# Kernel tuning notes

Measured on AMD Instinct MI355X. Metric: run time of the kernel, lower is better.

## Reference

```python
import jax, jax.numpy as jnp
import numpy as np
import math

E = 256      # emb_size
H = 4        # num_heads
D = E // H   # head_dim
EXPLORE_SCALE = 0.5
EXPLOIT_SCALE = 0.5
TEMP_MIN = 0.5
TEMP_MAX = 2.0


def setup_inputs() -> dict:
    key = jax.random.key(0)
    ks = jax.random.split(key, 12)
    B, S = 4, 2048
    his_emb = jax.random.normal(ks[0], (B, S, E), dtype=jnp.float32)
    src_key_padding_mask = jax.random.randint(ks[1], (B, S), 0, 2) > 0
    explore = jax.random.uniform(ks[2], (B, S), dtype=jnp.float32)
    exploit = jax.random.uniform(ks[3], (B, S), dtype=jnp.float32)
    scale = 1.0 / math.sqrt(E)
    Wq = jax.random.normal(ks[4], (E, E), dtype=jnp.float32) * scale
    bq = jnp.zeros((E,), dtype=jnp.float32)
    Wk = jax.random.normal(ks[5], (E, E), dtype=jnp.float32) * scale
    bk = jnp.zeros((E,), dtype=jnp.float32)
    Wv = jax.random.normal(ks[6], (E, E), dtype=jnp.float32) * scale
    bv = jnp.zeros((E,), dtype=jnp.float32)
    Wo = jax.random.normal(ks[7], (E, E), dtype=jnp.float32) * scale
    bo = jnp.zeros((E,), dtype=jnp.float32)
    return {"his_emb": his_emb, "src_key_padding_mask": src_key_padding_mask,
            "explore": explore, "exploit": exploit,
            "Wq": Wq, "bq": bq, "Wk": Wk, "bk": bk,
            "Wv": Wv, "bv": bv, "Wo": Wo, "bo": bo}


def reference(his_emb, src_key_padding_mask, explore, exploit,
              Wq, bq, Wk, bk, Wv, bv, Wo, bo):
    B, S, _ = his_emb.shape
    # projections -> [B, H, S, D]
    q = (his_emb @ Wq + bq).reshape(B, S, H, D).transpose(0, 2, 1, 3)
    k = (his_emb @ Wk + bk).reshape(B, S, H, D).transpose(0, 2, 1, 3)
    v = (his_emb @ Wv + bv).reshape(B, S, H, D).transpose(0, 2, 1, 3)
    logits = jnp.einsum('bhqd,bhkd->bhqk', q, k) / math.sqrt(D)
    attn_mask = src_key_padding_mask[:, None, None, :]  # [B,1,1,S] over keys
    logits = jnp.where(attn_mask, -1e16, logits)
    # per-query dynamic temperature
    temp = 1.0 + EXPLORE_SCALE * explore - EXPLOIT_SCALE * exploit  # [B,S]
    temp = jnp.clip(temp, TEMP_MIN, TEMP_MAX)
    temp = jnp.where(src_key_padding_mask, 1.0, temp)
    logits = logits / temp[:, None, :, None]
    probs = jax.nn.softmax(logits, axis=-1)
    probs = jnp.where(attn_mask, 0.0, probs)
    probs = probs / jnp.maximum(probs.sum(axis=-1, keepdims=True), 1e-8)
    out = jnp.einsum('bhqk,bhkd->bhqd', probs, v)
    out = out.transpose(0, 2, 1, 3).reshape(B, S, E)
    out = out @ Wo + bo
    return jnp.where(src_key_padding_mask[:, :, None], 0.0, out)
```

## Files before the change

kernel.cpp:

```cpp
#include <hip/hip_runtime.h>
#include <math.h>

#define B_ 4
#define S_ 2048
#define E_ 256
#define H_ 4
#define D_ 64
#define NROW (B_*S_)
#define NCH 2
#define CHK (S_/NCH)
#define NT (CHK/64)
#define LOG2E 1.4426950408889634f
#define NFM  (-17.312340490667562f)

typedef __attribute__((ext_vector_type(8)))  short short8;
typedef __attribute__((ext_vector_type(4)))  float floatx4;
typedef __attribute__((ext_vector_type(16))) float floatx16;

__device__ __forceinline__ short f2bf(float f){
    union{float f; unsigned u;} x; x.f = f;
    unsigned r = x.u + 0x7fffu + ((x.u>>16)&1u);
    return (short)(r>>16);
}
__device__ __forceinline__ unsigned cvtpk(float a, float b){
    unsigned r; asm("v_cvt_pk_bf16_f32 %0, %1, %2" : "=v"(r) : "v"(a), "v"(b)); return r;
}

__global__ __launch_bounds__(256) void prep(
    const float* __restrict__ W0, const float* __restrict__ W1,
    const float* __restrict__ W2, const float* __restrict__ W3,
    const float* __restrict__ X,
    short* __restrict__ T0, short* __restrict__ T1,
    short* __restrict__ T2, short* __restrict__ T3,
    short* __restrict__ Xb)
{
    __shared__ float L[64][65];
    const int t = threadIdx.x;
    if (blockIdx.x >= 16){
        const int cid = (blockIdx.x - 16) + 128*blockIdx.y;
        const float4* src = (const float4*)(X + (size_t)cid*4096 + t*16);
        short8 o0, o1; float4 u;
        u = src[0]; o0[0]=f2bf(u.x); o0[1]=f2bf(u.y); o0[2]=f2bf(u.z); o0[3]=f2bf(u.w);
        u = src[1]; o0[4]=f2bf(u.x); o0[5]=f2bf(u.y); o0[6]=f2bf(u.z); o0[7]=f2bf(u.w);
        u = src[2]; o1[0]=f2bf(u.x); o1[1]=f2bf(u.y); o1[2]=f2bf(u.z); o1[3]=f2bf(u.w);
        u = src[3]; o1[4]=f2bf(u.x); o1[5]=f2bf(u.y); o1[6]=f2bf(u.z); o1[7]=f2bf(u.w);
        short* dst = Xb + (size_t)cid*4096 + t*16;
        *(short8*)dst = o0; *(short8*)(dst+8) = o1;
        return;
    }
    const float* W = blockIdx.y==0?W0: blockIdx.y==1?W1: blockIdx.y==2?W2:W3;
    short*       T = blockIdx.y==0?T0: blockIdx.y==1?T1: blockIdx.y==2?T2:T3;
    const int k0 = (blockIdx.x>>2)*64, n0 = (blockIdx.x&3)*64;
    {
        int r = t>>2, c0 = (t&3)*16;
        const float4* p = (const float4*)(W + (size_t)(k0+r)*E_ + n0 + c0);
        #pragma unroll
        for (int j=0;j<4;++j){
            float4 u = p[j];
            L[r][c0+4*j]=u.x; L[r][c0+4*j+1]=u.y; L[r][c0+4*j+2]=u.z; L[r][c0+4*j+3]=u.w;
        }
    }
    __syncthreads();
    {
        int n = t>>2, kk0 = (t&3)*16;
        short8 o0, o1;
        #pragma unroll
        for(int j=0;j<8;++j) o0[j] = f2bf(L[kk0+j][n]);
        #pragma unroll
        for(int j=0;j<8;++j) o1[j] = f2bf(L[kk0+8+j][n]);
        short* dst = T + (size_t)(n0+n)*E_ + k0 + kk0;
        *(short8*)dst = o0; *(short8*)(dst+8) = o1;
    }
}

__global__ __launch_bounds__(256) void qkv_gemm(
    const short* __restrict__ Xb,
    const short* __restrict__ Wtq, const float* __restrict__ bq,
    const short* __restrict__ Wtk, const float* __restrict__ bk,
    const short* __restrict__ Wtv, const float* __restrict__ bv,
    short* __restrict__ Q, short* __restrict__ K, short* __restrict__ Vt)
{
    const int z = blockIdx.z;
    const short* Wt   = z==0?Wtq: z==1?Wtk:Wtv;
    const float* bias = z==0?bq:  z==1?bk:bv;

    __shared__ __align__(16) short As[64][72];
    __shared__ __align__(16) short Bs[64][72];

    const int t=threadIdx.x, w=t>>6, lane=t&63, ln=lane&15, quad=lane>>4;
    const int m0 = blockIdx.y*64, n0 = blockIdx.x*64;

    floatx4 acc[4] = {};
    for (int kt=0; kt<E_; kt+=64){
        __syncthreads();
        {
            int r=t>>2, c0=(t&3)*16;
            const uint4* pa = (const uint4*)(Xb + (size_t)(m0+r)*E_ + kt + c0);
            *(uint4*)&As[r][c0] = pa[0]; *(uint4*)&As[r][c0+8] = pa[1];
            const uint4* pb = (const uint4*)(Wt + (size_t)(n0+r)*E_ + kt + c0);
            *(uint4*)&Bs[r][c0] = pb[0]; *(uint4*)&Bs[r][c0+8] = pb[1];
        }
        __syncthreads();
        short8 a0 = *(const short8*)&As[w*16+ln][quad*8];
        short8 a1 = *(const short8*)&As[w*16+ln][32+quad*8];
        #pragma unroll
        for (int c=0;c<4;++c){
            short8 b0 = *(const short8*)&Bs[c*16+ln][quad*8];
            short8 b1 = *(const short8*)&Bs[c*16+ln][32+quad*8];
            acc[c] = __builtin_amdgcn_mfma_f32_16x16x32_bf16(a0,b0,acc[c],0,0,0);
            acc[c] = __builtin_amdgcn_mfma_f32_16x16x32_bf16(a1,b1,acc[c],0,0,0);
        }
    }
    if (z<2){
        short* dst = z==0?Q:K;
        #pragma unroll
        for(int c=0;c<4;++c){
            int colg = n0 + c*16 + ln;
            float bia = bias[colg];
            #pragma unroll
            for(int reg=0;reg<4;++reg){
                int row = m0 + w*16 + quad*4 + reg;
                dst[(size_t)row*E_ + colg] = f2bf(acc[c][reg] + bia);
            }
        }
    } else {
        #pragma unroll
        for(int c=0;c<4;++c){
            int colg = n0 + c*16 + ln;
            int hx = colg>>6, d = colg&63;
            float bia = bias[colg];
            #pragma unroll
            for(int reg=0;reg<4;++reg){
                int row = m0 + w*16 + quad*4 + reg;
                int bb = row>>11, s = row&(S_-1);
                Vt[((size_t)((bb*H_+hx)*D_+d))*S_ + s] = f2bf(acc[c][reg] + bia);
            }
        }
    }
}

__global__ __launch_bounds__(256) void attn_mfma(
    const short* __restrict__ Qb, const short* __restrict__ Kb, const short* __restrict__ Vtb,
    const int* __restrict__ mask,
    const float* __restrict__ explore, const float* __restrict__ exploit,
    float* __restrict__ OP, float* __restrict__ Lb)
{
    const int bid = blockIdx.x + 16*blockIdx.y + 32*blockIdx.z;
    const int swz = (bid & 7)*64 + (bid >> 3);
    const int bx = swz & 15;
    const int ck = (swz >> 4) & 1;
    const int z  = swz >> 5;
    const int b = z >> 2, h = z & 3;
    const int q0 = bx*128;
    const int k0 = ck*CHK;

    const int t = threadIdx.x, w = t>>6, lane = t&63, l31 = lane&31, hi = lane>>5;

    __shared__ __align__(16) short Ks[2][64][72];
    __shared__ __align__(16) short Vs[2][64][72];
    __shared__ float mb[2][64];

    const int qbase = q0 + w*32;
    const int qg = qbase + l31;
    float tsc2;
    {
        float ex = explore[b*S_+qg], xp = exploit[b*S_+qg];
        float tmp = fminf(fmaxf(1.0f + 0.5f*ex - 0.5f*xp, 0.5f), 2.0f);
        if (mask[b*S_+qg]) tmp = 1.0f;
        tsc2 = LOG2E/(tmp*8.0f);
    }
    const size_t qrow = (size_t)(b*S_+qg)*E_ + h*D_ + hi*8;
    const short8 qf0 = *(const short8*)(Qb + qrow);
    const short8 qf1 = *(const short8*)(Qb + qrow + 16);
    const short8 qf2 = *(const short8*)(Qb + qrow + 32);
    const short8 qf3 = *(const short8*)(Qb + qrow + 48);

    floatx16 ofa = {}, ofb = {};
    float lacc = 0.0f;

    const int sr = t>>2, sc = (t&3)*16;
    const short* kgp = Kb  + (size_t)(b*S_)*E_ + h*D_ + sc;
    const short* vgp = Vtb + ((size_t)(b*H_+h)*D_ + sr)*S_;

    uint4 rk0, rk1, rv0, rv1; float mfv = 0.0f;
    {
        const uint4* gk = (const uint4*)(kgp + (size_t)(k0+sr)*E_);
        rk0 = gk[0]; rk1 = gk[1];
        const uint4* gv = (const uint4*)(vgp + k0 + sc);
        rv0 = gv[0]; rv1 = gv[1];
        if (t < 64) mfv = mask[b*S_ + k0 + t] ? -1e30f : NFM;
    }
    *(uint4*)&Ks[0][sr][sc] = rk0; *(uint4*)&Ks[0][sr][sc+8] = rk1;
    *(uint4*)&Vs[0][sr][sc] = rv0; *(uint4*)&Vs[0][sr][sc+8] = rv1;
    if (t < 64) mb[0][t] = mfv;
    {
        const uint4* gk = (const uint4*)(kgp + (size_t)(k0+64+sr)*E_);
        rk0 = gk[0]; rk1 = gk[1];
        const uint4* gv = (const uint4*)(vgp + k0 + 64 + sc);
        rv0 = gv[0]; rv1 = gv[1];
        if (t < 64) mfv = mask[b*S_ + k0 + 64 + t] ? -1e30f : NFM;
    }
    __syncthreads();

    int cur = 0;
    #pragma unroll 1
    for (int it = 0; it < NT; ++it){
        const short (*Kc)[72] = Ks[cur];
        const short (*Vc)[72] = Vs[cur];
        #pragma unroll
        for (int kg = 0; kg < 2; ++kg){
            floatx16 st = {};
            const short8 kf0 = *(const short8*)&Kc[kg*32+l31][hi*8];
            const short8 kf1 = *(const short8*)&Kc[kg*32+l31][16+hi*8];
            const short8 kf2 = *(const short8*)&Kc[kg*32+l31][32+hi*8];
            const short8 kf3 = *(const short8*)&Kc[kg*32+l31][48+hi*8];
            __builtin_amdgcn_s_setprio(1);
            st = __builtin_amdgcn_mfma_f32_32x32x16_bf16(kf0, qf0, st, 0,0,0);
            st = __builtin_amdgcn_mfma_f32_32x32x16_bf16(kf1, qf1, st, 0,0,0);
            st = __builtin_amdgcn_mfma_f32_32x32x16_bf16(kf2, qf2, st, 0,0,0);
            st = __builtin_amdgcn_mfma_f32_32x32x16_bf16(kf3, qf3, st, 0,0,0);
            __builtin_amdgcn_s_setprio(0);
            const float4 m0_ = *(const float4*)&mb[cur][kg*32 +      4*hi];
            const float4 m1_ = *(const float4*)&mb[cur][kg*32 +  8 + 4*hi];
            const float4 m2_ = *(const float4*)&mb[cur][kg*32 + 16 + 4*hi];
            const float4 m3_ = *(const float4*)&mb[cur][kg*32 + 24 + 4*hi];
            const float mbf[16] = {m0_.x,m0_.y,m0_.z,m0_.w, m1_.x,m1_.y,m1_.z,m1_.w,
                                   m2_.x,m2_.y,m2_.z,m2_.w, m3_.x,m3_.y,m3_.z,m3_.w};
            float p[16];
            #pragma unroll
            for (int r = 0; r < 16; ++r){
                p[r] = __builtin_amdgcn_exp2f(st[r]*tsc2 + mbf[r]);
                lacc += p[r];
            }
            #pragma unroll
            for (int c = 0; c < 2; ++c){
                unsigned w0 = cvtpk(p[c*8+0], p[c*8+1]);
                unsigned w1 = cvtpk(p[c*8+2], p[c*8+3]);
                unsigned w2 = cvtpk(p[c*8+4], p[c*8+5]);
                unsigned w3 = cvtpk(p[c*8+6], p[c*8+7]);
                asm("v_permlane32_swap_b32 %0, %1" : "+v"(w0), "+v"(w2));
                asm("v_permlane32_swap_b32 %0, %1" : "+v"(w1), "+v"(w3));
                union { uint4 u; short8 s; } pc;
                pc.u.x = w0; pc.u.y = w1; pc.u.z = w2; pc.u.w = w3;
                const short8 vf0 = *(const short8*)&Vc[l31]   [kg*32 + c*16 + hi*8];
                const short8 vf1 = *(const short8*)&Vc[32+l31][kg*32 + c*16 + hi*8];
                __builtin_amdgcn_s_setprio(1);
                ofa = __builtin_amdgcn_mfma_f32_32x32x16_bf16(pc.s, vf0, ofa, 0,0,0);
                ofb = __builtin_amdgcn_mfma_f32_32x32x16_bf16(pc.s, vf1, ofb, 0,0,0);
                __builtin_amdgcn_s_setprio(0);
            }
        }
        if (it + 1 < NT){
            *(uint4*)&Ks[cur^1][sr][sc] = rk0; *(uint4*)&Ks[cur^1][sr][sc+8] = rk1;
            *(uint4*)&Vs[cur^1][sr][sc] = rv0; *(uint4*)&Vs[cur^1][sr][sc+8] = rv1;
            if (t < 64) mb[cur^1][t] = mfv;
            if (it + 2 < NT){
                const int kt2 = k0 + (it+2)*64;
                const uint4* gk = (const uint4*)(kgp + (size_t)(kt2+sr)*E_);
                rk0 = gk[0]; rk1 = gk[1];
                const uint4* gv = (const uint4*)(vgp + kt2 + sc);
                rv0 = gv[0]; rv1 = gv[1];
                if (t < 64) mfv = mask[b*S_ + kt2 + t] ? -1e30f : NFM;
            }
        }
        __syncthreads();
        cur ^= 1;
    }

    const float l = lacc + __shfl_xor(lacc, 32);
    const size_t obase = ((size_t)(ck*B_+b)*H_+h)*S_;
    if (hi == 0) Lb[obase + qg] = l;
    #pragma unroll
    for (int r = 0; r < 16; ++r){
        const int q = qbase + (r&3) + 8*(r>>2) + 4*hi;
        float* dst = OP + (obase + q)*D_;
        dst[l31]      = ofa[r];
        dst[32 + l31] = ofb[r];
    }
}

__global__ __launch_bounds__(256) void out_gemm(
    const float* __restrict__ OP, const float* __restrict__ Lb,
    const short* __restrict__ Wto, const float* __restrict__ bo,
    const int* __restrict__ mask, float* __restrict__ out)
{
    __shared__ __align__(16) short As[64][72];
    __shared__ __align__(16) short Bs[64][72];
    const int bid = blockIdx.x + 4*blockIdx.y;
    const int swz = (bid & 7)*64 + (bid >> 3);
    const int n0 = (swz & 3)*64;
    const int m0 = (swz >> 2)*64;
    const int t=threadIdx.x, w=t>>6, lane=t&63, ln=lane&15, quad=lane>>4;
    floatx4 acc[4] = {};
    const int sr=t>>2, sc=(t&3)*16;
    const int rowg = m0 + sr, bb = rowg>>11, ss = rowg&(S_-1);
    #pragma unroll 1
    for (int kt=0; kt<E_; kt+=64){
        const int hx = kt>>6;
        const size_t r0 = ((size_t)(bb)*H_+hx)*S_+ss;
        const size_t r1 = ((size_t)(B_+bb)*H_+hx)*S_+ss;
        const float lsum = Lb[r0] + Lb[r1];
        const float rl = 1.0f/fmaxf(lsum, 1e-8f);
        const float* pa0 = OP + r0*D_ + sc;
        const float* pa1 = OP + r1*D_ + sc;
        const float4 u0 = *(const float4*)(pa0+0), u1 = *(const float4*)(pa0+4),
                     u2 = *(const float4*)(pa0+8), u3 = *(const float4*)(pa0+12);
        const float4 v0 = *(const float4*)(pa1+0), v1 = *(const float4*)(pa1+4),
                     v2 = *(const float4*)(pa1+8), v3 = *(const float4*)(pa1+12);
        const uint4* pb = (const uint4*)(Wto + (size_t)(n0+sr)*E_ + kt + sc);
        const uint4 bw0 = pb[0], bw1 = pb[1];
        __syncthreads();
        union { uint4 u; short8 s; } cA, cB;
        cA.u.x = cvtpk((u0.x+v0.x)*rl, (u0.y+v0.y)*rl);
        cA.u.y = cvtpk((u0.z+v0.z)*rl, (u0.w+v0.w)*rl);
        cA.u.z = cvtpk((u1.x+v1.x)*rl, (u1.y+v1.y)*rl);
        cA.u.w = cvtpk((u1.z+v1.z)*rl, (u1.w+v1.w)*rl);
        cB.u.x = cvtpk((u2.x+v2.x)*rl, (u2.y+v2.y)*rl);
        cB.u.y = cvtpk((u2.z+v2.z)*rl, (u2.w+v2.w)*rl);
        cB.u.z = cvtpk((u3.x+v3.x)*rl, (u3.y+v3.y)*rl);
        cB.u.w = cvtpk((u3.z+v3.z)*rl, (u3.w+v3.w)*rl);
        *(short8*)&As[sr][sc]   = cA.s;
        *(short8*)&As[sr][sc+8] = cB.s;
        *(uint4*)&Bs[sr][sc] = bw0; *(uint4*)&Bs[sr][sc+8] = bw1;
        __syncthreads();
        const short8 a0 = *(const short8*)&As[w*16+ln][quad*8];
        const short8 a1 = *(const short8*)&As[w*16+ln][32+quad*8];
        #pragma unroll
        for (int c=0;c<4;++c){
            const short8 b0 = *(const short8*)&Bs[c*16+ln][quad*8];
            const short8 b1 = *(const short8*)&Bs[c*16+ln][32+quad*8];
            acc[c] = __builtin_amdgcn_mfma_f32_16x16x32_bf16(a0,b0,acc[c],0,0,0);
            acc[c] = __builtin_amdgcn_mfma_f32_16x16x32_bf16(a1,b1,acc[c],0,0,0);
        }
    }
    #pragma unroll
    for(int c=0;c<4;++c){
        const int colg = n0 + c*16 + ln;
        const float bia = bo[colg];
        #pragma unroll
        for(int reg=0;reg<4;++reg){
            const int row = m0 + w*16 + quad*4 + reg;
            out[(size_t)row*E_ + colg] = mask[row] ? 0.0f : (acc[c][reg] + bia);
        }
    }
}

extern "C" void kernel_launch(void* const* d_in, const int* in_sizes, int n_in,
                              void* d_out, int out_size, void* d_ws, size_t ws_size,
                              hipStream_t stream) {
    const float* his     = (const float*)d_in[0];
    const int*   mask    = (const int*)d_in[1];
    const float* explore = (const float*)d_in[2];
    const float* exploit = (const float*)d_in[3];
    const float* Wq = (const float*)d_in[4];
    const float* bq = (const float*)d_in[5];
    const float* Wk = (const float*)d_in[6];
    const float* bk = (const float*)d_in[7];
    const float* Wv = (const float*)d_in[8];
    const float* bv = (const float*)d_in[9];
    const float* Wo = (const float*)d_in[10];
    const float* bo = (const float*)d_in[11];

    char* ws = (char*)d_ws;
    const size_t NE2 = (size_t)NROW * E_ * 2;
    short* Wtq  = (short*)(ws);                    ws += E_*E_*2;
    short* Wtk  = (short*)(ws);                    ws += E_*E_*2;
    short* Wtv  = (short*)(ws);                    ws += E_*E_*2;
    short* Wto  = (short*)(ws);                    ws += E_*E_*2;
    short* Xb   = (short*)(ws);                    ws += NE2;
    short* Qb   = (short*)(ws);                    ws += NE2;
    short* Kb   = (short*)(ws);                    ws += NE2;
    short* Vtb  = (short*)(ws);                    ws += NE2;
    float* OP   = (float*)(ws);                    ws += (size_t)NCH*NROW*E_*4;
    float* Lb   = (float*)(ws);                    ws += (size_t)NCH*B_*H_*S_*4;

    prep<<<dim3(144,4), 256, 0, stream>>>(Wq, Wk, Wv, Wo, his, Wtq, Wtk, Wtv, Wto, Xb);

    qkv_gemm<<<dim3(E_/64, NROW/64, 3), 256, 0, stream>>>(
        Xb, Wtq, bq, Wtk, bk, Wtv, bv, Qb, Kb, Vtb);

    attn_mfma<<<dim3(S_/128, NCH, B_*H_), 256, 0, stream>>>(
        Qb, Kb, Vtb, mask, explore, exploit, OP, Lb);

    out_gemm<<<dim3(E_/64, NROW/64), 256, 0, stream>>>(OP, Lb, Wto, bo, mask, (float*)d_out);
}
```

Before: 132.2 us.

## Fuse all stages into one persistent kernel with software grid barriers

Merges the prep, QKV GEMM, attention and output GEMM kernels into a single 512-block persistent kernel whose phases are separated by an atomic-counter grid barrier, with a four-launch fallback if occupancy is too low. The attention phase now reads K and V fragments straight from global memory into registers instead of staging them through double-buffered LDS, and loads the whole key-mask chunk into LDS up front. The QKV phase has each block loop over Q, K and V serially. The aim is to remove launch gaps and the LDS staging cost. In exchange it adds barrier spin costs, a memset launch, a per-call occupancy query on the host, and a risk of deadlock if not all 512 blocks are co-resident.

```diff
diff --git a/kernel.cpp b/kernel.cpp
--- a/kernel.cpp
+++ b/kernel.cpp
@@ -10,6 +10,7 @@
 #define NCH 2
 #define CHK (S_/NCH)
 #define NT (CHK/64)
+#define NBLK 512
 #define LOG2E 1.4426950408889634f
 #define NFM  (-17.312340490667562f)
 
@@ -26,321 +27,319 @@
     unsigned r; asm("v_cvt_pk_bf16_f32 %0, %1, %2" : "=v"(r) : "v"(a), "v"(b)); return r;
 }
 
-__global__ __launch_bounds__(256) void prep(
-    const float* __restrict__ W0, const float* __restrict__ W1,
-    const float* __restrict__ W2, const float* __restrict__ W3,
-    const float* __restrict__ X,
-    short* __restrict__ T0, short* __restrict__ T1,
-    short* __restrict__ T2, short* __restrict__ T3,
-    short* __restrict__ Xb)
+__device__ __forceinline__ void gridbar(unsigned* bar){
+    __threadfence();
+    __syncthreads();
+    if (threadIdx.x == 0){
+        unsigned* cnt = bar;
+        unsigned* gen = bar + 1;
+        unsigned g = __hip_atomic_load(gen, __ATOMIC_ACQUIRE, __HIP_MEMORY_SCOPE_AGENT);
+        unsigned a = __hip_atomic_fetch_add(cnt, 1u, __ATOMIC_ACQ_REL, __HIP_MEMORY_SCOPE_AGENT);
+        if (a == (unsigned)(NBLK-1)){
+            __hip_atomic_store(cnt, 0u, __ATOMIC_RELAXED, __HIP_MEMORY_SCOPE_AGENT);
+            __hip_atomic_fetch_add(gen, 1u, __ATOMIC_RELEASE, __HIP_MEMORY_SCOPE_AGENT);
+        } else {
+            int spins = 0;
+            while (__hip_atomic_load(gen, __ATOMIC_ACQUIRE, __HIP_MEMORY_SCOPE_AGENT) == g){
+                __builtin_amdgcn_s_sleep(32);
+                if (++spins > (1<<16)) break;
+            }
+        }
+    }
+    __syncthreads();
+    __threadfence();
+}
+
+struct Prm {
+    const float* his; const int* mask; const float* explore; const float* exploit;
+    const float* Wq; const float* bq; const float* Wk; const float* bk;
+    const float* Wv; const float* bv; const float* Wo; const float* bo;
+    short* Wtq; short* Wtk; short* Wtv; short* Wto;
+    short* Xb; short* Qb; short* Kb; short* Vtb;
+    float* OP; float* Lb; unsigned* bar; float* out;
+};
+
+__global__ __launch_bounds__(256,2) void fused(Prm p, int phase)
 {
-    __shared__ float L[64][65];
-    const int t = threadIdx.x;
-    if (blockIdx.x >= 16){
-        const int cid = (blockIdx.x - 16) + 128*blockIdx.y;
-        const float4* src = (const float4*)(X + (size_t)cid*4096 + t*16);
-        short8 o0, o1; float4 u;
-        u = src[0]; o0[0]=f2bf(u.x); o0[1]=f2bf(u.y); o0[2]=f2bf(u.z); o0[3]=f2bf(u.w);
-        u = src[1]; o0[4]=f2bf(u.x); o0[5]=f2bf(u.y); o0[6]=f2bf(u.z); o0[7]=f2bf(u.w);
-        u = src[2]; o1[0]=f2bf(u.x); o1[1]=f2bf(u.y); o1[2]=f2bf(u.z); o1[3]=f2bf(u.w);
-        u = src[3]; o1[4]=f2bf(u.x); o1[5]=f2bf(u.y); o1[6]=f2bf(u.z); o1[7]=f2bf(u.w);
-        short* dst = Xb + (size_t)cid*4096 + t*16;
+    __shared__ __align__(16) char SMEM[22528];
+    short (*As)[72]  = (short(*)[72])SMEM;
+    short (*Bs)[72]  = (short(*)[72])(SMEM + 9216);
+    float (*Ltr)[65] = (float(*)[65])SMEM;
+    float* MBall     = (float*)(SMEM + 18432);
+    const int bid = blockIdx.x;
+    const int t   = threadIdx.x;
+
+    if (phase < 0 || phase == 0){
+        const int gtid = bid*256 + t;
+        const float4* src = (const float4*)p.his + (size_t)gtid*4;
+        short8 o0,o1; float4 u;
+        u=src[0]; o0[0]=f2bf(u.x); o0[1]=f2bf(u.y); o0[2]=f2bf(u.z); o0[3]=f2bf(u.w);
+        u=src[1]; o0[4]=f2bf(u.x); o0[5]=f2bf(u.y); o0[6]=f2bf(u.z); o0[7]=f2bf(u.w);
+        u=src[2]; o1[0]=f2bf(u.x); o1[1]=f2bf(u.y); o1[2]=f2bf(u.z); o1[3]=f2bf(u.w);
+        u=src[3]; o1[4]=f2bf(u.x); o1[5]=f2bf(u.y); o1[6]=f2bf(u.z); o1[7]=f2bf(u.w);
+        short* dst = p.Xb + (size_t)gtid*16;
         *(short8*)dst = o0; *(short8*)(dst+8) = o1;
-        return;
-    }
-    const float* W = blockIdx.y==0?W0: blockIdx.y==1?W1: blockIdx.y==2?W2:W3;
-    short*       T = blockIdx.y==0?T0: blockIdx.y==1?T1: blockIdx.y==2?T2:T3;
-    const int k0 = (blockIdx.x>>2)*64, n0 = (blockIdx.x&3)*64;
-    {
-        int r = t>>2, c0 = (t&3)*16;
-        const float4* p = (const float4*)(W + (size_t)(k0+r)*E_ + n0 + c0);
+        if (bid < 64){
+            const int wi = bid>>4, tile = bid&15;
+            const float* W = wi==0?p.Wq: wi==1?p.Wk: wi==2?p.Wv:p.Wo;
+            short*       T = wi==0?p.Wtq: wi==1?p.Wtk: wi==2?p.Wtv:p.Wto;
+            const int k0=(tile>>2)*64, n0=(tile&3)*64;
+            {
+                int r=t>>2, c0=(t&3)*16;
+                const float4* pp = (const float4*)(W + (size_t)(k0+r)*E_ + n0 + c0);
+                #pragma unroll
+                for (int j=0;j<4;++j){
+                    float4 v = pp[j];
+                    Ltr[r][c0+4*j]=v.x; Ltr[r][c0+4*j+1]=v.y; Ltr[r][c0+4*j+2]=v.z; Ltr[r][c0+4*j+3]=v.w;
+                }
+            }
+            __syncthreads();
+            {
+                int n=t>>2, kk0=(t&3)*16;
+                short8 t0, t1;
+                #pragma unroll
+                for(int j=0;j<8;++j) t0[j] = f2bf(Ltr[kk0+j][n]);
+                #pragma unroll
+                for(int j=0;j<8;++j) t1[j] = f2bf(Ltr[kk0+8+j][n]);
+                short* d2 = T + (size_t)(n0+n)*E_ + k0 + kk0;
+                *(short8*)d2 = t0; *(short8*)(d2+8) = t1;
+            }
+        }
+    }
+    if (phase < 0) gridbar(p.bar);
+
+    if (phase < 0 || phase == 1){
+        const int w=t>>6, lane=t&63, ln=lane&15, quad=lane>>4;
+        const int swz = (bid&7)*64 + (bid>>3);
+        const int n0 = (swz&3)*64, m0 = (swz>>2)*64;
+        const int sr=t>>2, sc=(t&3)*16;
+        #pragma unroll 1
+        for (int z=0; z<3; ++z){
+            const short* Wt   = z==0?p.Wtq: z==1?p.Wtk:p.Wtv;
+            const float* bias = z==0?p.bq:  z==1?p.bk:p.bv;
+            floatx4 acc[4] = {};
+            #pragma unroll 1
+            for (int kt=0; kt<E_; kt+=64){
+                __syncthreads();
+                {
+                    const uint4* pa = (const uint4*)(p.Xb + (size_t)(m0+sr)*E_ + kt + sc);
+                    *(uint4*)&As[sr][sc] = pa[0]; *(uint4*)&As[sr][sc+8] = pa[1];
+                    const uint4* pb = (const uint4*)(Wt + (size_t)(n0+sr)*E_ + kt + sc);
+                    *(uint4*)&Bs[sr][sc] = pb[0]; *(uint4*)&Bs[sr][sc+8] = pb[1];
+                }
+                __syncthreads();
+                short8 a0 = *(const short8*)&As[w*16+ln][quad*8];
+                short8 a1 = *(const short8*)&As[w*16+ln][32+quad*8];
+                #pragma unroll
+                for (int c=0;c<4;++c){
+                    short8 b0 = *(const short8*)&Bs[c*16+ln][quad*8];
+                    short8 b1 = *(const short8*)&Bs[c*16+ln][32+quad*8];
+                    acc[c] = __builtin_amdgcn_mfma_f32_16x16x32_bf16(a0,b0,acc[c],0,0,0);
+                    acc[c] = __builtin_amdgcn_mfma_f32_16x16x32_bf16(a1,b1,acc[c],0,0,0);
+                }
+            }
+            if (z<2){
+                short* dst = z==0?p.Qb:p.Kb;
+                #pragma unroll
+                for(int c=0;c<4;++c){
+                    int colg = n0 + c*16 + ln;
+                    float bia = bias[colg];
+                    #pragma unroll
+                    for(int reg=0;reg<4;++reg){
+                        int row = m0 + w*16 + quad*4 + reg;
+                        dst[(size_t)row*E_ + colg] = f2bf(acc[c][reg] + bia);
+                    }
+                }
+            } else {
+                #pragma unroll
+                for(int c=0;c<4;++c){
+                    int colg = n0 + c*16 + ln;
+                    int hx = colg>>6, d = colg&63;
+                    float bia = bias[colg];
+                    #pragma unroll
+                    for(int reg=0;reg<4;++reg){
+                        int row = m0 + w*16 + quad*4 + reg;
+                        int bb = row>>11, s = row&(S_-1);
+                        p.Vtb[((size_t)((bb*H_+hx)*D_+d))*S_ + s] = f2bf(acc[c][reg] + bia);
+                    }
+                }
+            }
+            __syncthreads();
+        }
+    }
+    if (phase < 0) gridbar(p.bar);
+
+    if (phase < 0 || phase == 2){
+        const int swz = (bid&7)*64 + (bid>>3);
+        const int bx = swz & 15;
+        const int ck = (swz>>4)&1;
+        const int z  = swz>>5;
+        const int b = z>>2, h = z&3;
+        const int q0 = bx*128, k0 = ck*CHK;
+        const int w = t>>6, lane = t&63, l31 = lane&31, hi = lane>>5;
+        const int qbase = q0 + w*32;
+        const int qg = qbase + l31;
+
         #pragma unroll
         for (int j=0;j<4;++j){
-            float4 u = p[j];
-            L[r][c0+4*j]=u.x; L[r][c0+4*j+1]=u.y; L[r][c0+4*j+2]=u.z; L[r][c0+4*j+3]=u.w;
-        }
-    }
-    __syncthreads();
-    {
-        int n = t>>2, kk0 = (t&3)*16;
-        short8 o0, o1;
+            int kk = t + j*256;
+            MBall[kk] = p.mask[b*S_ + k0 + kk] ? -1e30f : NFM;
+        }
+        float tsc2;
+        {
+            float ex = p.explore[b*S_+qg], xp = p.exploit[b*S_+qg];
+            float tmp = fminf(fmaxf(1.0f + 0.5f*ex - 0.5f*xp, 0.5f), 2.0f);
+            if (p.mask[b*S_+qg]) tmp = 1.0f;
+            tsc2 = LOG2E/(tmp*8.0f);
+        }
+        const size_t qrow = (size_t)(b*S_+qg)*E_ + h*D_ + hi*8;
+        const short8 qf0 = *(const short8*)(p.Qb + qrow);
+        const short8 qf1 = *(const short8*)(p.Qb + qrow + 16);
+        const short8 qf2 = *(const short8*)(p.Qb + qrow + 32);
+        const short8 qf3 = *(const short8*)(p.Qb + qrow + 48);
+        __syncthreads();
+
+        const short* kbase = p.Kb + (size_t)(b*S_)*E_ + h*D_ + hi*8;
+        const short* vbase = p.Vtb + ((size_t)((b*H_+h)*D_ + l31))*S_ + hi*8;
+
+        floatx16 ofa = {}, ofb = {};
+        float lacc = 0.0f;
+
+        short8 kA[4], kB[4];
+        {
+            const short* kb = kbase + (size_t)(k0 + l31)*E_;
+            kA[0]=*(const short8*)(kb); kA[1]=*(const short8*)(kb+16);
+            kA[2]=*(const short8*)(kb+32); kA[3]=*(const short8*)(kb+48);
+        }
+
+        #pragma unroll 1
+        for (int it = 0; it < NT; ++it){
+            const int kt = k0 + it*64;
+            {
+                const short* kb = kbase + (size_t)(kt + 32 + l31)*E_;
+                kB[0]=*(const short8*)(kb); kB[1]=*(const short8*)(kb+16);
+                kB[2]=*(const short8*)(kb+32); kB[3]=*(const short8*)(kb+48);
+            }
+            #pragma unroll
+            for (int kg = 0; kg < 2; ++kg){
+                const short8* kf = kg ? kB : kA;
+                floatx16 st = {};
+                __builtin_amdgcn_s_setprio(1);
+                st = __builtin_amdgcn_mfma_f32_32x32x16_bf16(kf[0], qf0, st, 0,0,0);
+                st = __builtin_amdgcn_mfma_f32_32x32x16_bf16(kf[1], qf1, st, 0,0,0);
+                st = __builtin_amdgcn_mfma_f32_32x32x16_bf16(kf[2], qf2, st, 0,0,0);
+                st = __builtin_amdgcn_mfma_f32_32x32x16_bf16(kf[3], qf3, st, 0,0,0);
+                __builtin_amdgcn_s_setprio(0);
+                if (kg == 1 && it + 1 < NT){
+                    const short* kb = kbase + (size_t)(kt + 64 + l31)*E_;
+                    kA[0]=*(const short8*)(kb); kA[1]=*(const short8*)(kb+16);
+                    kA[2]=*(const short8*)(kb+32); kA[3]=*(const short8*)(kb+48);
+                }
+                const short* vb = vbase + kt + kg*32;
+                const short8 vf0 = *(const short8*)(vb);
+                const short8 vf1 = *(const short8*)(vb + (size_t)32*S_);
+                const short8 vf2 = *(const short8*)(vb + 16);
+                const short8 vf3 = *(const short8*)(vb + 16 + (size_t)32*S_);
+                const int mbase = it*64 + kg*32 + 4*hi;
+                const float4 m0_ = *(const float4*)&MBall[mbase];
+                const float4 m1_ = *(const float4*)&MBall[mbase + 8];
+                const float4 m2_ = *(const float4*)&MBall[mbase + 16];
+                const float4 m3_ = *(const float4*)&MBall[mbase + 24];
+                const float mbf[16] = {m0_.x,m0_.y,m0_.z,m0_.w, m1_.x,m1_.y,m1_.z,m1_.w,
+                                       m2_.x,m2_.y,m2_.z,m2_.w, m3_.x,m3_.y,m3_.z,m3_.w};
+                float pr[16];
+                #pragma unroll
+                for (int r = 0; r < 16; ++r){
+                    pr[r] = __builtin_amdgcn_exp2f(st[r]*tsc2 + mbf[r]);
+                    lacc += pr[r];
+                }
+                #pragma unroll
+                for (int c = 0; c < 2; ++c){
+                    unsigned u0 = cvtpk(pr[c*8+0], pr[c*8+1]);
+                    unsigned u1 = cvtpk(pr[c*8+2], pr[c*8+3]);
+                    unsigned u2 = cvtpk(pr[c*8+4], pr[c*8+5]);
+                    unsigned u3 = cvtpk(pr[c*8+6], pr[c*8+7]);
+                    asm("v_permlane32_swap_b32 %0, %1" : "+v"(u0), "+v"(u2));
+                    asm("v_permlane32_swap_b32 %0, %1" : "+v"(u1), "+v"(u3));
+                    union { uint4 u; short8 s; } pc;
+                    pc.u.x = u0; pc.u.y = u1; pc.u.z = u2; pc.u.w = u3;
+                    __builtin_amdgcn_s_setprio(1);
+                    ofa = __builtin_amdgcn_mfma_f32_32x32x16_bf16(pc.s, c?vf2:vf0, ofa, 0,0,0);
+                    ofb = __builtin_amdgcn_mfma_f32_32x32x16_bf16(pc.s, c?vf3:vf1, ofb, 0,0,0);
+                    __builtin_amdgcn_s_setprio(0);
+                }
+            }
+        }
+
+        const float l = lacc + __shfl_xor(lacc, 32);
+        const size_t obase = ((size_t)(ck*B_+b)*H_+h)*S_;
+        if (hi == 0) p.Lb[obase + qg] = l;
         #pragma unroll
-        for(int j=0;j<8;++j) o0[j] = f2bf(L[kk0+j][n]);
-        #pragma unroll
-        for(int j=0;j<8;++j) o1[j] = f2bf(L[kk0+8+j][n]);
-        short* dst = T + (size_t)(n0+n)*E_ + k0 + kk0;
-        *(short8*)dst = o0; *(short8*)(dst+8) = o1;
-    }
-}
-
-__global__ __launch_bounds__(256) void qkv_gemm(
-    const short* __restrict__ Xb,
-    const short* __restrict__ Wtq, const float* __restrict__ bq,
-    const short* __restrict__ Wtk, const float* __restrict__ bk,
-    const short* __restrict__ Wtv, const float* __restrict__ bv,
-    short* __restrict__ Q, short* __restrict__ K, short* __restrict__ Vt)
-{
-    const int z = blockIdx.z;
-    const short* Wt   = z==0?Wtq: z==1?Wtk:Wtv;
-    const float* bias = z==0?bq:  z==1?bk:bv;
-
-    __shared__ __align__(16) short As[64][72];
-    __shared__ __align__(16) short Bs[64][72];
-
-    const int t=threadIdx.x, w=t>>6, lane=t&63, ln=lane&15, quad=lane>>4;
-    const int m0 = blockIdx.y*64, n0 = blockIdx.x*64;
-
-    floatx4 acc[4] = {};
-    for (int kt=0; kt<E_; kt+=64){
-        __syncthreads();
-        {
-            int r=t>>2, c0=(t&3)*16;
-            const uint4* pa = (const uint4*)(Xb + (size_t)(m0+r)*E_ + kt + c0);
-            *(uint4*)&As[r][c0] = pa[0]; *(uint4*)&As[r][c0+8] = pa[1];
-            const uint4* pb = (const uint4*)(Wt + (size_t)(n0+r)*E_ + kt + c0);
-            *(uint4*)&Bs[r][c0] = pb[0]; *(uint4*)&Bs[r][c0+8] = pb[1];
-        }
-        __syncthreads();
-        short8 a0 = *(const short8*)&As[w*16+ln][quad*8];
-        short8 a1 = *(const short8*)&As[w*16+ln][32+quad*8];
-        #pragma unroll
-        for (int c=0;c<4;++c){
-            short8 b0 = *(const short8*)&Bs[c*16+ln][quad*8];
-            short8 b1 = *(const short8*)&Bs[c*16+ln][32+quad*8];
-            acc[c] = __builtin_amdgcn_mfma_f32_16x16x32_bf16(a0,b0,acc[c],0,0,0);
-            acc[c] = __builtin_amdgcn_mfma_f32_16x16x32_bf16(a1,b1,acc[c],0,0,0);
-        }
-    }
-    if (z<2){
-        short* dst = z==0?Q:K;
+        for (int r = 0; r < 16; ++r){
+            const int q = qbase + (r&3) + 8*(r>>2) + 4*hi;
+            float* dst = p.OP + (obase + q)*D_;
+            dst[l31]      = ofa[r];
+            dst[32 + l31] = ofb[r];
+        }
+    }
+    if (phase < 0) gridbar(p.bar);
+
+    if (phase < 0 || phase == 3){
+        const int swz = (bid&7)*64 + (bid>>3);
+        const int n0 = (swz & 3)*64;
+        const int m0 = (swz >> 2)*64;
+        const int w=t>>6, lane=t&63, ln=lane&15, quad=lane>>4;
+        floatx4 acc[4] = {};
+        const int sr=t>>2, sc=(t&3)*16;
+        const int rowg = m0 + sr, bb = rowg>>11, ss = rowg&(S_-1);
+        #pragma unroll 1
+        for (int kt=0; kt<E_; kt+=64){
+            const int hx = kt>>6;
+            const size_t r0 = ((size_t)(bb)*H_+hx)*S_+ss;
+            const size_t r1 = ((size_t)(B_+bb)*H_+hx)*S_+ss;
+            const float lsum = p.Lb[r0] + p.Lb[r1];
+            const float rl = 1.0f/fmaxf(lsum, 1e-8f);
+            const float* pa0 = p.OP + r0*D_ + sc;
+            const float* pa1 = p.OP + r1*D_ + sc;
+            const float4 u0 = *(const float4*)(pa0+0), u1 = *(const float4*)(pa0+4),
+                         u2 = *(const float4*)(pa0+8), u3 = *(const float4*)(pa0+12);
+            const float4 v0 = *(const float4*)(pa1+0), v1 = *(const float4*)(pa1+4),
+                         v2 = *(const float4*)(pa1+8), v3 = *(const float4*)(pa1+12);
+            const uint4* pb = (const uint4*)(p.Wto + (size_t)(n0+sr)*E_ + kt + sc);
+            const uint4 bw0 = pb[0], bw1 = pb[1];
+            __syncthreads();
+            union { uint4 u; short8 s; } cA, cB;
+            cA.u.x = cvtpk((u0.x+v0.x)*rl, (u0.y+v0.y)*rl);
+            cA.u.y = cvtpk((u0.z+v0.z)*rl, (u0.w+v0.w)*rl);
+            cA.u.z = cvtpk((u1.x+v1.x)*rl, (u1.y+v1.y)*rl);
+            cA.u.w = cvtpk((u1.z+v1.z)*rl, (u1.w+v1.w)*rl);
+            cB.u.x = cvtpk((u2.x+v2.x)*rl, (u2.y+v2.y)*rl);
+            cB.u.y = cvtpk((u2.z+v2.z)*rl, (u2.w+v2.w)*rl);
+            cB.u.z = cvtpk((u3.x+v3.x)*rl, (u3.y+v3.y)*rl);
+            cB.u.w = cvtpk((u3.z+v3.z)*rl, (u3.w+v3.w)*rl);
+            *(short8*)&As[sr][sc]   = cA.s;
+            *(short8*)&As[sr][sc+8] = cB.s;
+            *(uint4*)&Bs[sr][sc] = bw0; *(uint4*)&Bs[sr][sc+8] = bw1;
+            __syncthreads();
+            const short8 a0 = *(const short8*)&As[w*16+ln][quad*8];
+            const short8 a1 = *(const short8*)&As[w*16+ln][32+quad*8];
+            #pragma unroll
+            for (int c=0;c<4;++c){
+                const short8 b0 = *(const short8*)&Bs[c*16+ln][quad*8];
+                const short8 b1 = *(const short8*)&Bs[c*16+ln][32+quad*8];
+                acc[c] = __builtin_amdgcn_mfma_f32_16x16x32_bf16(a0,b0,acc[c],0,0,0);
+                acc[c] = __builtin_amdgcn_mfma_f32_16x16x32_bf16(a1,b1,acc[c],0,0,0);
+            }
+        }
         #pragma unroll
         for(int c=0;c<4;++c){
-            int colg = n0 + c*16 + ln;
-            float bia = bias[colg];
+            const int colg = n0 + c*16 + ln;
+            const float bia = p.bo[colg];
             #pragma unroll
             for(int reg=0;reg<4;++reg){
-                int row = m0 + w*16 + quad*4 + reg;
-                dst[(size_t)row*E_ + colg] = f2bf(acc[c][reg] + bia);
-            }
-        }
-    } else {
-        #pragma unroll
-        for(int c=0;c<4;++c){
-            int colg = n0 + c*16 + ln;
-            int hx = colg>>6, d = colg&63;
-            float bia = bias[colg];
-            #pragma unroll
-            for(int reg=0;reg<4;++reg){
-                int row = m0 + w*16 + quad*4 + reg;
-                int bb = row>>11, s = row&(S_-1);
-                Vt[((size_t)((bb*H_+hx)*D_+d))*S_ + s] = f2bf(acc[c][reg] + bia);
-            }
-        }
-    }
-}
-
-__global__ __launch_bounds__(256) void attn_mfma(
-    const short* __restrict__ Qb, const short* __restrict__ Kb, const short* __restrict__ Vtb,
-    const int* __restrict__ mask,
-    const float* __restrict__ explore, const float* __restrict__ exploit,
-    float* __restrict__ OP, float* __restrict__ Lb)
-{
-    const int bid = blockIdx.x + 16*blockIdx.y + 32*blockIdx.z;
-    const int swz = (bid & 7)*64 + (bid >> 3);
-    const int bx = swz & 15;
-    const int ck = (swz >> 4) & 1;
-    const int z  = swz >> 5;
-    const int b = z >> 2, h = z & 3;
-    const int q0 = bx*128;
-    const int k0 = ck*CHK;
-
-    const int t = threadIdx.x, w = t>>6, lane = t&63, l31 = lane&31, hi = lane>>5;
-
-    __shared__ __align__(16) short Ks[2][64][72];
-    __shared__ __align__(16) short Vs[2][64][72];
-    __shared__ float mb[2][64];
-
-    const int qbase = q0 + w*32;
-    const int qg = qbase + l31;
-    float tsc2;
-    {
-        float ex = explore[b*S_+qg], xp = exploit[b*S_+qg];
-        float tmp = fminf(fmaxf(1.0f + 0.5f*ex - 0.5f*xp, 0.5f), 2.0f);
-        if (mask[b*S_+qg]) tmp = 1.0f;
-        tsc2 = LOG2E/(tmp*8.0f);
-    }
-    const size_t qrow = (size_t)(b*S_+qg)*E_ + h*D_ + hi*8;
-    const short8 qf0 = *(const short8*)(Qb + qrow);
-    const short8 qf1 = *(const short8*)(Qb + qrow + 16);
-    const short8 qf2 = *(const short8*)(Qb + qrow + 32);
-    const short8 qf3 = *(const short8*)(Qb + qrow + 48);
-
-    floatx16 ofa = {}, ofb = {};
-    float lacc = 0.0f;
-
-    const int sr = t>>2, sc = (t&3)*16;
-    const short* kgp = Kb  + (size_t)(b*S_)*E_ + h*D_ + sc;
-    const short* vgp = Vtb + ((size_t)(b*H_+h)*D_ + sr)*S_;
-
-    uint4 rk0, rk1, rv0, rv1; float mfv = 0.0f;
-    {
-        const uint4* gk = (const uint4*)(kgp + (size_t)(k0+sr)*E_);
-        rk0 = gk[0]; rk1 = gk[1];
-        const uint4* gv = (const uint4*)(vgp + k0 + sc);
-        rv0 = gv[0]; rv1 = gv[1];
-        if (t < 64) mfv = mask[b*S_ + k0 + t] ? -1e30f : NFM;
-    }
-    *(uint4*)&Ks[0][sr][sc] = rk0; *(uint4*)&Ks[0][sr][sc+8] = rk1;
-    *(uint4*)&Vs[0][sr][sc] = rv0; *(uint4*)&Vs[0][sr][sc+8] = rv1;
-    if (t < 64) mb[0][t] = mfv;
-    {
-        const uint4* gk = (const uint4*)(kgp + (size_t)(k0+64+sr)*E_);
-        rk0 = gk[0]; rk1 = gk[1];
-        const uint4* gv = (const uint4*)(vgp + k0 + 64 + sc);
-        rv0 = gv[0]; rv1 = gv[1];
-        if (t < 64) mfv = mask[b*S_ + k0 + 64 + t] ? -1e30f : NFM;
-    }
-    __syncthreads();
-
-    int cur = 0;
-    #pragma unroll 1
-    for (int it = 0; it < NT; ++it){
-        const short (*Kc)[72] = Ks[cur];
-        const short (*Vc)[72] = Vs[cur];
-        #pragma unroll
-        for (int kg = 0; kg < 2; ++kg){
-            floatx16 st = {};
-            const short8 kf0 = *(const short8*)&Kc[kg*32+l31][hi*8];
-            const short8 kf1 = *(const short8*)&Kc[kg*32+l31][16+hi*8];
-            const short8 kf2 = *(const short8*)&Kc[kg*32+l31][32+hi*8];
-            const short8 kf3 = *(const short8*)&Kc[kg*32+l31][48+hi*8];
-            __builtin_amdgcn_s_setprio(1);
-            st = __builtin_amdgcn_mfma_f32_32x32x16_bf16(kf0, qf0, st, 0,0,0);
-            st = __builtin_amdgcn_mfma_f32_32x32x16_bf16(kf1, qf1, st, 0,0,0);
-            st = __builtin_amdgcn_mfma_f32_32x32x16_bf16(kf2, qf2, st, 0,0,0);
-            st = __builtin_amdgcn_mfma_f32_32x32x16_bf16(kf3, qf3, st, 0,0,0);
-            __builtin_amdgcn_s_setprio(0);
-            const float4 m0_ = *(const float4*)&mb[cur][kg*32 +      4*hi];
-            const float4 m1_ = *(const float4*)&mb[cur][kg*32 +  8 + 4*hi];
-            const float4 m2_ = *(const float4*)&mb[cur][kg*32 + 16 + 4*hi];
-            const float4 m3_ = *(const float4*)&mb[cur][kg*32 + 24 + 4*hi];
-            const float mbf[16] = {m0_.x,m0_.y,m0_.z,m0_.w, m1_.x,m1_.y,m1_.z,m1_.w,
-                                   m2_.x,m2_.y,m2_.z,m2_.w, m3_.x,m3_.y,m3_.z,m3_.w};
-            float p[16];
-            #pragma unroll
-            for (int r = 0; r < 16; ++r){
-                p[r] = __builtin_amdgcn_exp2f(st[r]*tsc2 + mbf[r]);
-                lacc += p[r];
-            }
-            #pragma unroll
-            for (int c = 0; c < 2; ++c){
-                unsigned w0 = cvtpk(p[c*8+0], p[c*8+1]);
-                unsigned w1 = cvtpk(p[c*8+2], p[c*8+3]);
-                unsigned w2 = cvtpk(p[c*8+4], p[c*8+5]);
-                unsigned w3 = cvtpk(p[c*8+6], p[c*8+7]);
-                asm("v_permlane32_swap_b32 %0, %1" : "+v"(w0), "+v"(w2));
-                asm("v_permlane32_swap_b32 %0, %1" : "+v"(w1), "+v"(w3));
-                union { uint4 u; short8 s; } pc;
-                pc.u.x = w0; pc.u.y = w1; pc.u.z = w2; pc.u.w = w3;
-                const short8 vf0 = *(const short8*)&Vc[l31]   [kg*32 + c*16 + hi*8];
-                const short8 vf1 = *(const short8*)&Vc[32+l31][kg*32 + c*16 + hi*8];
-                __builtin_amdgcn_s_setprio(1);
-                ofa = __builtin_amdgcn_mfma_f32_32x32x16_bf16(pc.s, vf0, ofa, 0,0,0);
-                ofb = __builtin_amdgcn_mfma_f32_32x32x16_bf16(pc.s, vf1, ofb, 0,0,0);
-                __builtin_amdgcn_s_setprio(0);
-            }
-        }
-        if (it + 1 < NT){
-            *(uint4*)&Ks[cur^1][sr][sc] = rk0; *(uint4*)&Ks[cur^1][sr][sc+8] = rk1;
-            *(uint4*)&Vs[cur^1][sr][sc] = rv0; *(uint4*)&Vs[cur^1][sr][sc+8] = rv1;
-            if (t < 64) mb[cur^1][t] = mfv;
-            if (it + 2 < NT){
-                const int kt2 = k0 + (it+2)*64;
-                const uint4* gk = (const uint4*)(kgp + (size_t)(kt2+sr)*E_);
-                rk0 = gk[0]; rk1 = gk[1];
-                const uint4* gv = (const uint4*)(vgp + kt2 + sc);
-                rv0 = gv[0]; rv1 = gv[1];
-                if (t < 64) mfv = mask[b*S_ + kt2 + t] ? -1e30f : NFM;
-            }
-        }
-        __syncthreads();
-        cur ^= 1;
-    }
-
-    const float l = lacc + __shfl_xor(lacc, 32);
-    const size_t obase = ((size_t)(ck*B_+b)*H_+h)*S_;
-    if (hi == 0) Lb[obase + qg] = l;
-    #pragma unroll
-    for (int r = 0; r < 16; ++r){
-        const int q = qbase + (r&3) + 8*(r>>2) + 4*hi;
-        float* dst = OP + (obase + q)*D_;
-        dst[l31]      = ofa[r];
-        dst[32 + l31] = ofb[r];
-    }
-}
-
-__global__ __launch_bounds__(256) void out_gemm(
-    const float* __restrict__ OP, const float* __restrict__ Lb,
-    const short* __restrict__ Wto, const float* __restrict__ bo,
-    const int* __restrict__ mask, float* __restrict__ out)
-{
-    __shared__ __align__(16) short As[64][72];
-    __shared__ __align__(16) short Bs[64][72];
-    const int bid = blockIdx.x + 4*blockIdx.y;
-    const int swz = (bid & 7)*64 + (bid >> 3);
-    const int n0 = (swz & 3)*64;
-    const int m0 = (swz >> 2)*64;
-    const int t=threadIdx.x, w=t>>6, lane=t&63, ln=lane&15, quad=lane>>4;
-    floatx4 acc[4] = {};
-    const int sr=t>>2, sc=(t&3)*16;
-    const int rowg = m0 + sr, bb = rowg>>11, ss = rowg&(S_-1);
-    #pragma unroll 1
-    for (int kt=0; kt<E_; kt+=64){
-        const int hx = kt>>6;
-        const size_t r0 = ((size_t)(bb)*H_+hx)*S_+ss;
-        const size_t r1 = ((size_t)(B_+bb)*H_+hx)*S_+ss;
-        const float lsum = Lb[r0] + Lb[r1];
-        const float rl = 1.0f/fmaxf(lsum, 1e-8f);
-        const float* pa0 = OP + r0*D_ + sc;
-        const float* pa1 = OP + r1*D_ + sc;
-        const float4 u0 = *(const float4*)(pa0+0), u1 = *(const float4*)(pa0+4),
-                     u2 = *(const float4*)(pa0+8), u3 = *(const float4*)(pa0+12);
-        const float4 v0 = *(const float4*)(pa1+0), v1 = *(const float4*)(pa1+4),
-                     v2 = *(const float4*)(pa1+8), v3 = *(const float4*)(pa1+12);
-        const uint4* pb = (const uint4*)(Wto + (size_t)(n0+sr)*E_ + kt + sc);
-        const uint4 bw0 = pb[0], bw1 = pb[1];
-        __syncthreads();
-        union { uint4 u; short8 s; } cA, cB;
-        cA.u.x = cvtpk((u0.x+v0.x)*rl, (u0.y+v0.y)*rl);
-        cA.u.y = cvtpk((u0.z+v0.z)*rl, (u0.w+v0.w)*rl);
-        cA.u.z = cvtpk((u1.x+v1.x)*rl, (u1.y+v1.y)*rl);
-        cA.u.w = cvtpk((u1.z+v1.z)*rl, (u1.w+v1.w)*rl);
-        cB.u.x = cvtpk((u2.x+v2.x)*rl, (u2.y+v2.y)*rl);
-        cB.u.y = cvtpk((u2.z+v2.z)*rl, (u2.w+v2.w)*rl);
-        cB.u.z = cvtpk((u3.x+v3.x)*rl, (u3.y+v3.y)*rl);
-        cB.u.w = cvtpk((u3.z+v3.z)*rl, (u3.w+v3.w)*rl);
-        *(short8*)&As[sr][sc]   = cA.s;
-        *(short8*)&As[sr][sc+8] = cB.s;
-        *(uint4*)&Bs[sr][sc] = bw0; *(uint4*)&Bs[sr][sc+8] = bw1;
-        __syncthreads();
-        const short8 a0 = *(const short8*)&As[w*16+ln][quad*8];
-        const short8 a1 = *(const short8*)&As[w*16+ln][32+quad*8];
-        #pragma unroll
-        for (int c=0;c<4;++c){
-            const short8 b0 = *(const short8*)&Bs[c*16+ln][quad*8];
-            const short8 b1 = *(const short8*)&Bs[c*16+ln][32+quad*8];
-            acc[c] = __builtin_amdgcn_mfma_f32_16x16x32_bf16(a0,b0,acc[c],0,0,0);
-            acc[c] = __builtin_amdgcn_mfma_f32_16x16x32_bf16(a1,b1,acc[c],0,0,0);
-        }
-    }
-    #pragma unroll
-    for(int c=0;c<4;++c){
-        const int colg = n0 + c*16 + ln;
-        const float bia = bo[colg];
-        #pragma unroll
-        for(int reg=0;reg<4;++reg){
-            const int row = m0 + w*16 + quad*4 + reg;
-            out[(size_t)row*E_ + colg] = mask[row] ? 0.0f : (acc[c][reg] + bia);
+                const int row = m0 + w*16 + quad*4 + reg;
+                p.out[(size_t)row*E_ + colg] = p.mask[row] ? 0.0f : (acc[c][reg] + bia);
+            }
         }
     }
 }
@@ -348,39 +347,41 @@
 extern "C" void kernel_launch(void* const* d_in, const int* in_sizes, int n_in,
                               void* d_out, int out_size, void* d_ws, size_t ws_size,
                               hipStream_t stream) {
-    const float* his     = (const float*)d_in[0];
-    const int*   mask    = (const int*)d_in[1];
-    const float* explore = (const float*)d_in[2];
-    const float* exploit = (const float*)d_in[3];
-    const float* Wq = (const float*)d_in[4];
-    const float* bq = (const float*)d_in[5];
-    const float* Wk = (const float*)d_in[6];
-    const float* bk = (const float*)d_in[7];
-    const float* Wv = (const float*)d_in[8];
-    const float* bv = (const float*)d_in[9];
-    const float* Wo = (const float*)d_in[10];
-    const float* bo = (const float*)d_in[11];
-
     char* ws = (char*)d_ws;
     const size_t NE2 = (size_t)NROW * E_ * 2;
-    short* Wtq  = (short*)(ws);                    ws += E_*E_*2;
-    short* Wtk  = (short*)(ws);                    ws += E_*E_*2;
-    short* Wtv  = (short*)(ws);                    ws += E_*E_*2;
-    short* Wto  = (short*)(ws);                    ws += E_*E_*2;
-    short* Xb   = (short*)(ws);                    ws += NE2;
-    short* Qb   = (short*)(ws);                    ws += NE2;
-    short* Kb   = (short*)(ws);                    ws += NE2;
-    short* Vtb  = (short*)(ws);                    ws += NE2;
-    float* OP   = (float*)(ws);                    ws += (size_t)NCH*NROW*E_*4;
-    float* Lb   = (float*)(ws);                    ws += (size_t)NCH*B_*H_*S_*4;
-
-    prep<<<dim3(144,4), 256, 0, stream>>>(Wq, Wk, Wv, Wo, his, Wtq, Wtk, Wtv, Wto, Xb);
-
-    qkv_gemm<<<dim3(E_/64, NROW/64, 3), 256, 0, stream>>>(
-        Xb, Wtq, bq, Wtk, bk, Wtv, bv, Qb, Kb, Vtb);
-
-    attn_mfma<<<dim3(S_/128, NCH, B_*H_), 256, 0, stream>>>(
-        Qb, Kb, Vtb, mask, explore, exploit, OP, Lb);
-
-    out_gemm<<<dim3(E_/64, NROW/64), 256, 0, stream>>>(OP, Lb, Wto, bo, mask, (float*)d_out);
-}
+    Prm p;
+    p.his     = (const float*)d_in[0];
+    p.mask    = (const int*)d_in[1];
+    p.explore = (const float*)d_in[2];
+    p.exploit = (const float*)d_in[3];
+    p.Wq = (const float*)d_in[4];  p.bq = (const float*)d_in[5];
+    p.Wk = (const float*)d_in[6];  p.bk = (const float*)d_in[7];
+    p.Wv = (const float*)d_in[8];  p.bv = (const float*)d_in[9];
+    p.Wo = (const float*)d_in[10]; p.bo = (const float*)d_in[11];
+    p.Wtq = (short*)ws; ws += E_*E_*2;
+    p.Wtk = (short*)ws; ws += E_*E_*2;
+    p.Wtv = (short*)ws; ws += E_*E_*2;
+    p.Wto = (short*)ws; ws += E_*E_*2;
+    p.Xb  = (short*)ws; ws += NE2;
+    p.Qb  = (short*)ws; ws += NE2;
+    p.Kb  = (short*)ws; ws += NE2;
+    p.Vtb = (short*)ws; ws += NE2;
+    p.OP  = (float*)ws; ws += (size_t)NCH*NROW*E_*4;
+    p.Lb  = (float*)ws; ws += (size_t)NCH*B_*H_*S_*4;
+    p.bar = (unsigned*)ws; ws += 256;
+    p.out = (float*)d_out;
+
+    int maxb = 0;
+    hipError_t qerr = hipOccupancyMaxActiveBlocksPerMultiprocessor(&maxb, fused, 256, 0);
+    const bool coop = (qerr == hipSuccess && maxb >= 2);
+
+    if (coop){
+        hipMemsetAsync(p.bar, 0, 64, stream);
+        fused<<<dim3(NBLK), dim3(256), 0, stream>>>(p, -1);
+    } else {
+        fused<<<dim3(NBLK), dim3(256), 0, stream>>>(p, 0);
+        fused<<<dim3(NBLK), dim3(256), 0, stream>>>(p, 1);
+        fused<<<dim3(NBLK), dim3(256), 0, stream>>>(p, 2);
+        fused<<<dim3(NBLK), dim3(256), 0, stream>>>(p, 3);
+    }
+}
```

Result: slower. 170.6 us (+29.0%).
